# Optimization experiments

Measured on AMD Instinct MI355X. Metric: run time of the kernel, lower is better.

The kernel has to match this reference:

```python
import jax, jax.numpy as jnp
import numpy as np

jax.config.update("jax_enable_x64", True)  # torch lfilter runs in double precision

SR = 24000
RES_SIZE = 64
R_MIN, R_MAX = 0.9999, 0.99999
B, T = 4, 120000


def setup_inputs() -> dict:
    # Probe coefficients (fixed buffers, computed exactly as in Probe.__init__)
    theta_min = 2 * np.pi * 10.0 / SR
    theta_max = 2 * np.pi * 100.0 / SR
    theta = np.exp(np.linspace(np.log(theta_min), np.log(theta_max), RES_SIZE))
    radii = np.linspace(R_MIN, R_MAX, RES_SIZE)
    a1 = -2.0 * radii * np.cos(theta)          # [C]
    a2 = radii ** 2                             # [C]
    b0 = (1.0 - radii) * 0.5                    # [C]

    # Tank mixing weight: orthogonal init, shape [out=64, in=128] (rows orthonormal)
    rng = np.random.default_rng(1337)
    q, _ = np.linalg.qr(rng.standard_normal((2 * RES_SIZE, RES_SIZE)))  # [128,64], orthonormal cols
    W = q.T.astype(np.float32)                  # [64,128]

    key = jax.random.key(0)
    k1, k2 = jax.random.split(key)
    pred = jax.random.normal(k1, (B, 1, T), dtype=jnp.float32)
    target = jax.random.normal(k2, (B, 1, T), dtype=jnp.float32)
    return {
        "pred": pred,
        "target": target,
        "a1": jnp.asarray(a1, jnp.float64),
        "a2": jnp.asarray(a2, jnp.float64),
        "b0": jnp.asarray(b0, jnp.float64),
        "W": jnp.asarray(W, jnp.float32),
    }


def _biquad_bank(x, a1, a2, b0):
    """Biquad filter bank. x: [N, T] float64; coeffs: [C]. Returns [N, C, T].
    y[t] = b0*x[t] - a1*y[t-1] - a2*y[t-2]  (a0 = 1, b1 = b2 = 0, clamp=False)
    """
    n = x.shape[0]
    c = a1.shape[0]

    def step(carry, xt):
        y1, y2 = carry  # each [N, C]
        y = b0[None, :] * xt[:, None] - a1[None, :] * y1 - a2[None, :] * y2
        return (y, y1), y

    init = (jnp.zeros((n, c), x.dtype), jnp.zeros((n, c), x.dtype))
    _, ys = jax.lax.scan(step, init, x.T)      # [T, N, C]
    return jnp.transpose(ys, (1, 2, 0))        # [N, C, T]


def _probe(x, a1, a2, b0):
    """x: [B,1,T] float -> [B, 2C, T] float32 (fwd state ++ bwd state)."""
    xs = x[:, 0, :].astype(jnp.float64)        # [B, T]
    # run forward-time and reversed-time filters in one batched scan
    both = jnp.concatenate([xs, xs[:, ::-1]], axis=0)       # [2B, T]
    ys = _biquad_bank(both, a1, a2, b0)                      # [2B, C, T]
    nb = xs.shape[0]
    fwd_state = ys[:nb]                                      # [B, C, T]
    bwd_state = ys[nb:][:, :, ::-1]                          # [B, C, T] (flipped back)
    return jnp.concatenate([fwd_state, bwd_state], axis=1).astype(jnp.float32)


def _tank(x, W):
    """x: [B, 2C, T], W: [C, 2C] -> tanh(W @ x): [B, C, T]."""
    return jnp.tanh(jnp.einsum("bct,oc->bot", x, W))


def reference(pred, target, a1, a2, b0, W):
    t = pred.shape[-1]
    margin = t // 3
    p_emb = _tank(_probe(pred, a1, a2, b0), W)    # [B, C, T]
    t_emb = _tank(_probe(target, a1, a2, b0), W)  # [B, C, T]
    p_valid = p_emb[..., margin:t - margin]
    t_valid = t_emb[..., margin:t - margin]
    return jnp.mean(jnp.abs(p_valid - t_valid))
```

## Files before the change

### kernel.cpp

```cpp
#include <hip/hip_runtime.h>

#define T_LEN 120000
#define LBLK 160
#define PBLK 750
#define SEG_LEN 25
#define NSEG 30
#define CCH 32
#define NCHUNK (LBLK / CCH)
#define BATCH 4
#define K0 250
#define NKV 250
#define IB_LO 250
#define IB_HI 500
#define DENOM 20480000.0
#define YSTR 130

typedef _Float16 half8 __attribute__((ext_vector_type(8)));
typedef float f32x4 __attribute__((ext_vector_type(4)));

__device__ __forceinline__ float fast_tanh(float x) {
  float e = __expf(2.0f * x);
  return 1.0f - 2.0f / (e + 1.0f);
}

__device__ __forceinline__ void mat_pow(double A1, double A2, int e,
                                        double& r00, double& r01,
                                        double& r10, double& r11) {
  double m00 = -A1, m01 = -A2, m10 = 1.0, m11 = 0.0;
  r00 = 1.0; r01 = 0.0; r10 = 0.0; r11 = 1.0;
  while (e) {
    if (e & 1) {
      double t00 = r00 * m00 + r01 * m10, t01 = r00 * m01 + r01 * m11;
      double t10 = r10 * m00 + r11 * m10, t11 = r10 * m01 + r11 * m11;
      r00 = t00; r01 = t01; r10 = t10; r11 = t11;
    }
    e >>= 1;
    if (e) {
      double t00 = m00 * m00 + m01 * m10, t01 = m00 * m01 + m01 * m11;
      double t10 = m10 * m00 + m11 * m10, t11 = m10 * m01 + m11 * m11;
      m00 = t00; m01 = t01; m10 = t10; m11 = t11;
    }
  }
}

__global__ __launch_bounds__(256) void canon(
    const void* a1p, const void* a2p, const void* b0p, const float* __restrict__ W,
    double* ca1, double* ca2, double* cb0, float* cf, _Float16* Wh, double* wsum)
{
  int tid = threadIdx.x;
  __shared__ int isf64;
  if (tid == 0) {
    double probe = *(const double*)a2p;
    isf64 = (probe > 0.9 && probe < 1.0) ? 1 : 0;
    *wsum = 0.0;
  }
  __syncthreads();
  if (tid < 64) {
    double A1, A2, B0;
    if (isf64) {
      A1 = ((const double*)a1p)[tid];
      A2 = ((const double*)a2p)[tid];
      B0 = ((const double*)b0p)[tid];
    } else {
      A1 = (double)((const float*)a1p)[tid];
      A2 = (double)((const float*)a2p)[tid];
      B0 = (double)((const float*)b0p)[tid];
    }
    ca1[tid] = A1; ca2[tid] = A2; cb0[tid] = B0;
    cf[tid] = (float)A1; cf[64 + tid] = (float)A2;
    cf[128 + tid] = (float)B0; cf[192 + tid] = (float)(1.0 / A2);
  }
  for (int idx = tid; idx < 64 * 128; idx += 256) Wh[idx] = (_Float16)W[idx];
}

__global__ __launch_bounds__(64) void pass1(
    const float* __restrict__ pred, const float* __restrict__ tgt,
    const float* __restrict__ cf, double* __restrict__ fbuf)
{
  int k = blockIdx.x, r = blockIdx.y;
  int i = r >> 3, d = (r >> 2) & 1, b = r & 3;
  const float* sig = (i ? tgt : pred) + b * T_LEN;
  __shared__ float xs[LBLK];
  int base = k * LBLK;
  for (int j = threadIdx.x; j < LBLK; j += 64)
    xs[j] = d ? sig[T_LEN - 1 - (base + j)] : sig[base + j];
  __syncthreads();
  int ch = threadIdx.x;
  float A1 = cf[ch], A2 = cf[64 + ch], B0 = cf[128 + ch];
  float y1 = 0.0f, y2 = 0.0f;
  for (int j = 0; j < LBLK; ++j) {
    float y = fmaf(-A1, y1, fmaf(-A2, y2, B0 * xs[j]));
    y2 = y1; y1 = y;
  }
  int s = r * 64 + ch;
  ((double2*)fbuf)[(size_t)k * 1024 + s] = make_double2((double)y1, (double)y2);
}

__global__ __launch_bounds__(64) void pass2a(
    const double* __restrict__ a1, const double* __restrict__ a2,
    const double* __restrict__ fbuf, double* __restrict__ sbuf)
{
  int seg = blockIdx.x >> 4;
  int s = ((blockIdx.x & 15) << 6) + threadIdx.x;
  int ch = s & 63;
  double r00, r01, r10, r11;
  mat_pow(a1[ch], a2[ch], LBLK, r00, r01, r10, r11);
  const double2* fb = (const double2*)fbuf;
  double y1 = 0.0, y2 = 0.0;
  for (int jj = 0; jj < SEG_LEN / 5; ++jj) {
    size_t kb = (size_t)(seg * SEG_LEN + jj * 5) * 1024 + s;
    double2 f0 = fb[kb], f1 = fb[kb + 1024], f2 = fb[kb + 2048],
            f3 = fb[kb + 3072], f4 = fb[kb + 4096];
    double n1, n2;
    n1 = r00*y1 + r01*y2 + f0.x; n2 = r10*y1 + r11*y2 + f0.y; y1=n1; y2=n2;
    n1 = r00*y1 + r01*y2 + f1.x; n2 = r10*y1 + r11*y2 + f1.y; y1=n1; y2=n2;
    n1 = r00*y1 + r01*y2 + f2.x; n2 = r10*y1 + r11*y2 + f2.y; y1=n1; y2=n2;
    n1 = r00*y1 + r01*y2 + f3.x; n2 = r10*y1 + r11*y2 + f3.y; y1=n1; y2=n2;
    n1 = r00*y1 + r01*y2 + f4.x; n2 = r10*y1 + r11*y2 + f4.y; y1=n1; y2=n2;
  }
  ((double2*)sbuf)[(size_t)seg * 1024 + s] = make_double2(y1, y2);
}

__global__ __launch_bounds__(256) void pass2b(
    const double* __restrict__ a1, const double* __restrict__ a2,
    const double* __restrict__ sbuf, double* __restrict__ tbuf)
{
  int s = blockIdx.x * 256 + threadIdx.x;
  int ch = s & 63;
  double r00, r01, r10, r11;
  mat_pow(a1[ch], a2[ch], LBLK * SEG_LEN, r00, r01, r10, r11);
  const double2* sb = (const double2*)sbuf;
  double2* tb = (double2*)tbuf;
  double y1 = 0.0, y2 = 0.0;
  for (int seg = 0; seg < NSEG; ++seg) {
    tb[(size_t)seg * 1024 + s] = make_double2(y1, y2);
    double2 f = sb[(size_t)seg * 1024 + s];
    double n1 = r00 * y1 + r01 * y2 + f.x;
    double n2 = r10 * y1 + r11 * y2 + f.y;
    y1 = n1; y2 = n2;
  }
}

__global__ __launch_bounds__(64) void pass2c(
    const double* __restrict__ a1, const double* __restrict__ a2,
    const double* __restrict__ fbuf, const double* __restrict__ tbuf,
    double* __restrict__ ibuf)
{
  int seg = 10 + (blockIdx.x >> 4);
  int s = ((blockIdx.x & 15) << 6) + threadIdx.x;
  int ch = s & 63;
  double r00, r01, r10, r11;
  mat_pow(a1[ch], a2[ch], LBLK, r00, r01, r10, r11);
  const double2* fb = (const double2*)fbuf;
  double2* ib = (double2*)ibuf;
  double2 v = ((const double2*)tbuf)[(size_t)seg * 1024 + s];
  double y1 = v.x, y2 = v.y;
  for (int j = 0; j < SEG_LEN; ++j) {
    int k = seg * SEG_LEN + j;
    if (k >= IB_LO && k <= IB_HI)
      ib[(size_t)(k - IB_LO) * 1024 + s] = make_double2(y1, y2);
    double2 f = fb[(size_t)k * 1024 + s];
    double n1 = r00 * y1 + r01 * y2 + f.x;
    double n2 = r10 * y1 + r11 * y2 + f.y;
    y1 = n1; y2 = n2;
  }
}

__global__ __launch_bounds__(256, 4) void pass3(
    const float* __restrict__ pred, const float* __restrict__ tgt,
    const float* __restrict__ cf, const _Float16* __restrict__ Wh,
    const double* __restrict__ ibuf, double* __restrict__ wsum)
{
  int k = K0 + blockIdx.x;
  int b = blockIdx.y;
  int tid = threadIdx.x;
  __shared__ __align__(16) _Float16 ys[2][64 * YSTR];
  __shared__ float xs[2][LBLK];
  __shared__ float red[4];

  for (int idx = tid; idx < 2 * LBLK; idx += 256) {
    int ii = idx / LBLK, j = idx - ii * LBLK;
    const float* sig = (ii ? tgt : pred) + b * T_LEN;
    xs[ii][j] = sig[k * LBLK + j];
  }

  int g = tid >> 6, lane = tid & 63;
  int i = g >> 1, d = g & 1, ch = lane;
  int gu = __builtin_amdgcn_readfirstlane(g);
  int n0 = gu * 16;
  int lm = lane & 15, quad = lane >> 4;

  half8 wf[4][4];
  #pragma unroll
  for (int m0 = 0; m0 < 4; ++m0) {
    #pragma unroll
    for (int k0 = 0; k0 < 4; ++k0)
      wf[m0][k0] = *(const half8*)(Wh + (m0 * 16 + lm) * 128 + k0 * 32 + quad * 8);
  }

  int s = (i * 8 + d * 4 + b) * 64 + ch;
  float A1 = cf[ch], A2 = cf[64 + ch], B0 = cf[128 + ch], IA2 = cf[192 + ch];
  double2 v = (d == 0)
      ? ((const double2*)ibuf)[(size_t)(k - IB_LO) * 1024 + s]
      : ((const double2*)ibuf)[(size_t)(IB_HI - k) * 1024 + s];
  float st0 = (float)v.x, st1 = (float)v.y;
  __syncthreads();

  float loss = 0.0f;
  for (int cc = 0; cc < NCHUNK; ++cc) {
    _Float16* yb = ys[cc & 1];
    if (d == 0) {
      #pragma unroll
      for (int tt = 0; tt < CCH; ++tt) {
        float x = xs[i][cc * CCH + tt];
        float y = fmaf(-A1, st0, fmaf(-A2, st1, B0 * x));
        yb[(2 * tt + i) * YSTR + ch] = (_Float16)y;
        st1 = st0; st0 = y;
      }
    } else {
      #pragma unroll
      for (int tt = 0; tt < CCH; ++tt) {
        float x = xs[i][cc * CCH + tt];
        yb[(2 * tt + i) * YSTR + 64 + ch] = (_Float16)st0;
        float ym2 = (fmaf(-A1, st1, B0 * x) - st0) * IA2;
        st0 = st1; st1 = ym2;
      }
    }
    __syncthreads();

    const _Float16* yrow = &yb[(n0 + lm) * YSTR + quad * 8];
    half8 bf0 = *(const half8*)(yrow);
    half8 bf1 = *(const half8*)(yrow + 32);
    half8 bf2 = *(const half8*)(yrow + 64);
    half8 bf3 = *(const half8*)(yrow + 96);
    #pragma unroll
    for (int m0 = 0; m0 < 4; ++m0) {
      f32x4 c = {0.f, 0.f, 0.f, 0.f};
      c = __builtin_amdgcn_mfma_f32_16x16x32_f16(wf[m0][0], bf0, c, 0, 0, 0);
      c = __builtin_amdgcn_mfma_f32_16x16x32_f16(wf[m0][1], bf1, c, 0, 0, 0);
      c = __builtin_amdgcn_mfma_f32_16x16x32_f16(wf[m0][2], bf2, c, 0, 0, 0);
      c = __builtin_amdgcn_mfma_f32_16x16x32_f16(wf[m0][3], bf3, c, 0, 0, 0);
      #pragma unroll
      for (int r = 0; r < 4; ++r) {
        float vv = fast_tanh(c[r]);
        float p = __shfl_xor(vv, 1);
        loss += fabsf(vv - p);
      }
    }
  }

  #pragma unroll
  for (int off = 32; off > 0; off >>= 1) loss += __shfl_down(loss, off);
  if ((tid & 63) == 0) red[tid >> 6] = loss;
  __syncthreads();
  if (tid == 0) atomicAdd(wsum, (double)(red[0] + red[1] + red[2] + red[3]));
}

__global__ void finalize(const double* __restrict__ wsum, float* __restrict__ out) {
  out[0] = (float)(wsum[0] / DENOM);
}

extern "C" void kernel_launch(void* const* d_in, const int* in_sizes, int n_in,
                              void* d_out, int out_size, void* d_ws, size_t ws_size,
                              hipStream_t stream) {
  const float* pred = (const float*)d_in[0];
  const float* tgt  = (const float*)d_in[1];
  const float* W    = (const float*)d_in[5];
  float* out = (float*)d_out;

  double* base = (double*)d_ws;
  double* wsum = base;
  double* ca1  = base + 8;
  double* ca2  = base + 72;
  double* cb0  = base + 136;
  float*  cf   = (float*)(base + 200);
  _Float16* Wh = (_Float16*)(base + 328);
  double* fbuf = base + 2376;
  double* ibuf = fbuf + (size_t)PBLK * 1024 * 2;
  double* sbuf = ibuf + (size_t)(IB_HI - IB_LO + 1) * 1024 * 2;
  double* tbuf = sbuf + (size_t)NSEG * 1024 * 2;

  canon<<<1, 256, 0, stream>>>(d_in[2], d_in[3], d_in[4], W,
                               ca1, ca2, cb0, cf, Wh, wsum);
  pass1<<<dim3(PBLK, 16), 64, 0, stream>>>(pred, tgt, cf, fbuf);
  pass2a<<<NSEG * 16, 64, 0, stream>>>(ca1, ca2, fbuf, sbuf);
  pass2b<<<dim3(4), 256, 0, stream>>>(ca1, ca2, sbuf, tbuf);
  pass2c<<<11 * 16, 64, 0, stream>>>(ca1, ca2, fbuf, tbuf, ibuf);
  pass3<<<dim3(NKV, BATCH), 256, 0, stream>>>(pred, tgt, cf, Wh, ibuf, wsum);
  finalize<<<1, 1, 0, stream>>>(wsum, out);
}
```

Measured before the change: 137.1 us.

## Drop canon and pass2c kernels, fold state fix-up and coefficient conversion into pass3

Removes the coefficient canonicalisation kernel and the pass2c intermediate-state kernel. Each consumer now reads and converts the a1/a2/b0 coefficients itself, and pass3 rebuilds its starting state from the segment-start state plus up to 24 block-level matrix steps over fbuf. W is converted to fp16 directly inside pass3, and x is read from global memory instead of being staged in LDS. pass2b now batches its loads into two groups of 15. This cuts two kernel launches and their serial dependencies, at the cost of redundant per-block double-precision work in pass3 and uncoalesced-ish global x reads.

```diff
diff --git a/kernel.cpp b/kernel.cpp
--- a/kernel.cpp
+++ b/kernel.cpp
@@ -10,8 +10,6 @@
 #define BATCH 4
 #define K0 250
 #define NKV 250
-#define IB_LO 250
-#define IB_HI 500
 #define DENOM 20480000.0
 #define YSTR 130
 
@@ -21,6 +19,14 @@
 __device__ __forceinline__ float fast_tanh(float x) {
   float e = __expf(2.0f * x);
   return 1.0f - 2.0f / (e + 1.0f);
+}
+
+__device__ __forceinline__ bool coeffs_are_f64(const void* a2p) {
+  double probe = *(const double*)a2p;
+  return probe > 0.9 && probe < 1.0;
+}
+__device__ __forceinline__ double coeff_d(const void* p, bool f64, int ch) {
+  return f64 ? ((const double*)p)[ch] : (double)((const float*)p)[ch];
 }
 
 __device__ __forceinline__ void mat_pow(double A1, double A2, int e,
@@ -43,39 +49,10 @@
   }
 }
 
-__global__ __launch_bounds__(256) void canon(
-    const void* a1p, const void* a2p, const void* b0p, const float* __restrict__ W,
-    double* ca1, double* ca2, double* cb0, float* cf, _Float16* Wh, double* wsum)
-{
-  int tid = threadIdx.x;
-  __shared__ int isf64;
-  if (tid == 0) {
-    double probe = *(const double*)a2p;
-    isf64 = (probe > 0.9 && probe < 1.0) ? 1 : 0;
-    *wsum = 0.0;
-  }
-  __syncthreads();
-  if (tid < 64) {
-    double A1, A2, B0;
-    if (isf64) {
-      A1 = ((const double*)a1p)[tid];
-      A2 = ((const double*)a2p)[tid];
-      B0 = ((const double*)b0p)[tid];
-    } else {
-      A1 = (double)((const float*)a1p)[tid];
-      A2 = (double)((const float*)a2p)[tid];
-      B0 = (double)((const float*)b0p)[tid];
-    }
-    ca1[tid] = A1; ca2[tid] = A2; cb0[tid] = B0;
-    cf[tid] = (float)A1; cf[64 + tid] = (float)A2;
-    cf[128 + tid] = (float)B0; cf[192 + tid] = (float)(1.0 / A2);
-  }
-  for (int idx = tid; idx < 64 * 128; idx += 256) Wh[idx] = (_Float16)W[idx];
-}
-
 __global__ __launch_bounds__(64) void pass1(
     const float* __restrict__ pred, const float* __restrict__ tgt,
-    const float* __restrict__ cf, double* __restrict__ fbuf)
+    const void* a1p, const void* a2p, const void* b0p,
+    double* __restrict__ fbuf)
 {
   int k = blockIdx.x, r = blockIdx.y;
   int i = r >> 3, d = (r >> 2) & 1, b = r & 3;
@@ -86,7 +63,10 @@
     xs[j] = d ? sig[T_LEN - 1 - (base + j)] : sig[base + j];
   __syncthreads();
   int ch = threadIdx.x;
-  float A1 = cf[ch], A2 = cf[64 + ch], B0 = cf[128 + ch];
+  bool f64 = coeffs_are_f64(a2p);
+  float A1 = (float)coeff_d(a1p, f64, ch);
+  float A2 = (float)coeff_d(a2p, f64, ch);
+  float B0 = (float)coeff_d(b0p, f64, ch);
   float y1 = 0.0f, y2 = 0.0f;
   for (int j = 0; j < LBLK; ++j) {
     float y = fmaf(-A1, y1, fmaf(-A2, y2, B0 * xs[j]));
@@ -97,14 +77,15 @@
 }
 
 __global__ __launch_bounds__(64) void pass2a(
-    const double* __restrict__ a1, const double* __restrict__ a2,
+    const void* a1p, const void* a2p,
     const double* __restrict__ fbuf, double* __restrict__ sbuf)
 {
   int seg = blockIdx.x >> 4;
   int s = ((blockIdx.x & 15) << 6) + threadIdx.x;
   int ch = s & 63;
+  bool f64 = coeffs_are_f64(a2p);
   double r00, r01, r10, r11;
-  mat_pow(a1[ch], a2[ch], LBLK, r00, r01, r10, r11);
+  mat_pow(coeff_d(a1p, f64, ch), coeff_d(a2p, f64, ch), LBLK, r00, r01, r10, r11);
   const double2* fb = (const double2*)fbuf;
   double y1 = 0.0, y2 = 0.0;
   for (int jj = 0; jj < SEG_LEN / 5; ++jj) {
@@ -122,106 +103,117 @@
 }
 
 __global__ __launch_bounds__(256) void pass2b(
-    const double* __restrict__ a1, const double* __restrict__ a2,
+    const void* a1p, const void* a2p,
     const double* __restrict__ sbuf, double* __restrict__ tbuf)
 {
   int s = blockIdx.x * 256 + threadIdx.x;
   int ch = s & 63;
+  bool f64 = coeffs_are_f64(a2p);
   double r00, r01, r10, r11;
-  mat_pow(a1[ch], a2[ch], LBLK * SEG_LEN, r00, r01, r10, r11);
+  mat_pow(coeff_d(a1p, f64, ch), coeff_d(a2p, f64, ch), LBLK * SEG_LEN,
+          r00, r01, r10, r11);
   const double2* sb = (const double2*)sbuf;
   double2* tb = (double2*)tbuf;
   double y1 = 0.0, y2 = 0.0;
-  for (int seg = 0; seg < NSEG; ++seg) {
-    tb[(size_t)seg * 1024 + s] = make_double2(y1, y2);
-    double2 f = sb[(size_t)seg * 1024 + s];
-    double n1 = r00 * y1 + r01 * y2 + f.x;
-    double n2 = r10 * y1 + r11 * y2 + f.y;
-    y1 = n1; y2 = n2;
-  }
-}
-
-__global__ __launch_bounds__(64) void pass2c(
-    const double* __restrict__ a1, const double* __restrict__ a2,
-    const double* __restrict__ fbuf, const double* __restrict__ tbuf,
-    double* __restrict__ ibuf)
-{
-  int seg = 10 + (blockIdx.x >> 4);
-  int s = ((blockIdx.x & 15) << 6) + threadIdx.x;
-  int ch = s & 63;
-  double r00, r01, r10, r11;
-  mat_pow(a1[ch], a2[ch], LBLK, r00, r01, r10, r11);
-  const double2* fb = (const double2*)fbuf;
-  double2* ib = (double2*)ibuf;
-  double2 v = ((const double2*)tbuf)[(size_t)seg * 1024 + s];
-  double y1 = v.x, y2 = v.y;
-  for (int j = 0; j < SEG_LEN; ++j) {
-    int k = seg * SEG_LEN + j;
-    if (k >= IB_LO && k <= IB_HI)
-      ib[(size_t)(k - IB_LO) * 1024 + s] = make_double2(y1, y2);
-    double2 f = fb[(size_t)k * 1024 + s];
-    double n1 = r00 * y1 + r01 * y2 + f.x;
-    double n2 = r10 * y1 + r11 * y2 + f.y;
-    y1 = n1; y2 = n2;
+  #pragma unroll 1
+  for (int half = 0; half < 2; ++half) {
+    int base = half * 15;
+    double2 f[15];
+    #pragma unroll
+    for (int q = 0; q < 15; ++q) f[q] = sb[(size_t)(base + q) * 1024 + s];
+    #pragma unroll
+    for (int q = 0; q < 15; ++q) {
+      tb[(size_t)(base + q) * 1024 + s] = make_double2(y1, y2);
+      double n1 = r00 * y1 + r01 * y2 + f[q].x;
+      double n2 = r10 * y1 + r11 * y2 + f[q].y;
+      y1 = n1; y2 = n2;
+    }
   }
 }
 
 __global__ __launch_bounds__(256, 4) void pass3(
     const float* __restrict__ pred, const float* __restrict__ tgt,
-    const float* __restrict__ cf, const _Float16* __restrict__ Wh,
-    const double* __restrict__ ibuf, double* __restrict__ wsum)
+    const void* a1p, const void* a2p, const void* b0p,
+    const float* __restrict__ W, const double* __restrict__ fbuf,
+    const double* __restrict__ tbuf, double* __restrict__ wsum)
 {
   int k = K0 + blockIdx.x;
   int b = blockIdx.y;
   int tid = threadIdx.x;
   __shared__ __align__(16) _Float16 ys[2][64 * YSTR];
-  __shared__ float xs[2][LBLK];
   __shared__ float red[4];
 
-  for (int idx = tid; idx < 2 * LBLK; idx += 256) {
-    int ii = idx / LBLK, j = idx - ii * LBLK;
-    const float* sig = (ii ? tgt : pred) + b * T_LEN;
-    xs[ii][j] = sig[k * LBLK + j];
-  }
-
   int g = tid >> 6, lane = tid & 63;
-  int i = g >> 1, d = g & 1, ch = lane;
   int gu = __builtin_amdgcn_readfirstlane(g);
+  int iu = gu >> 1, du = gu & 1;
+  int ch = lane;
   int n0 = gu * 16;
   int lm = lane & 15, quad = lane >> 4;
+
+  bool f64 = coeffs_are_f64(a2p);
+  double A1d = coeff_d(a1p, f64, ch), A2d = coeff_d(a2p, f64, ch);
+  double B0d = coeff_d(b0p, f64, ch);
+  float A1 = (float)A1d, A2 = (float)A2d, B0 = (float)B0d;
+  float IA2 = (float)(1.0 / A2d);
+
+  int m = du ? (PBLK - k) : k;
+  int seg = m / SEG_LEN, j = m - seg * SEG_LEN;
+  int s = (iu * 8 + du * 4 + b) * 64 + ch;
+  double r00, r01, r10, r11;
+  mat_pow(A1d, A2d, LBLK, r00, r01, r10, r11);
+  double2 v0 = ((const double2*)tbuf)[(size_t)seg * 1024 + s];
+  double y1 = v0.x, y2 = v0.y;
+  const double2* fb = (const double2*)fbuf + (size_t)(seg * SEG_LEN) * 1024 + s;
+  #pragma unroll 1
+  for (int bb = 0; bb < 24; bb += 8) {
+    double2 f[8];
+    #pragma unroll
+    for (int q = 0; q < 8; ++q) f[q] = fb[(size_t)(bb + q) * 1024];
+    #pragma unroll
+    for (int q = 0; q < 8; ++q) {
+      if (bb + q < j) {
+        double n1 = r00 * y1 + r01 * y2 + f[q].x;
+        double n2 = r10 * y1 + r11 * y2 + f[q].y;
+        y1 = n1; y2 = n2;
+      }
+    }
+  }
+  float st0 = (float)y1, st1 = (float)y2;
 
   half8 wf[4][4];
   #pragma unroll
   for (int m0 = 0; m0 < 4; ++m0) {
     #pragma unroll
-    for (int k0 = 0; k0 < 4; ++k0)
-      wf[m0][k0] = *(const half8*)(Wh + (m0 * 16 + lm) * 128 + k0 * 32 + quad * 8);
-  }
-
-  int s = (i * 8 + d * 4 + b) * 64 + ch;
-  float A1 = cf[ch], A2 = cf[64 + ch], B0 = cf[128 + ch], IA2 = cf[192 + ch];
-  double2 v = (d == 0)
-      ? ((const double2*)ibuf)[(size_t)(k - IB_LO) * 1024 + s]
-      : ((const double2*)ibuf)[(size_t)(IB_HI - k) * 1024 + s];
-  float st0 = (float)v.x, st1 = (float)v.y;
-  __syncthreads();
+    for (int k0 = 0; k0 < 4; ++k0) {
+      const float* wp = W + (m0 * 16 + lm) * 128 + k0 * 32 + quad * 8;
+      float4 wa = *(const float4*)wp, wb = *(const float4*)(wp + 4);
+      half8 h;
+      h[0] = (_Float16)wa.x; h[1] = (_Float16)wa.y;
+      h[2] = (_Float16)wa.z; h[3] = (_Float16)wa.w;
+      h[4] = (_Float16)wb.x; h[5] = (_Float16)wb.y;
+      h[6] = (_Float16)wb.z; h[7] = (_Float16)wb.w;
+      wf[m0][k0] = h;
+    }
+  }
+
+  const float* xp = (iu ? tgt : pred) + b * T_LEN + k * LBLK;
 
   float loss = 0.0f;
   for (int cc = 0; cc < NCHUNK; ++cc) {
     _Float16* yb = ys[cc & 1];
-    if (d == 0) {
+    if (du == 0) {
       #pragma unroll
       for (int tt = 0; tt < CCH; ++tt) {
-        float x = xs[i][cc * CCH + tt];
+        float x = xp[cc * CCH + tt];
         float y = fmaf(-A1, st0, fmaf(-A2, st1, B0 * x));
-        yb[(2 * tt + i) * YSTR + ch] = (_Float16)y;
+        yb[(2 * tt + iu) * YSTR + ch] = (_Float16)y;
         st1 = st0; st0 = y;
       }
     } else {
       #pragma unroll
       for (int tt = 0; tt < CCH; ++tt) {
-        float x = xs[i][cc * CCH + tt];
-        yb[(2 * tt + i) * YSTR + 64 + ch] = (_Float16)st0;
+        float x = xp[cc * CCH + tt];
+        yb[(2 * tt + iu) * YSTR + 64 + ch] = (_Float16)st0;
         float ym2 = (fmaf(-A1, st1, B0 * x) - st0) * IA2;
         st0 = st1; st1 = ym2;
       }
@@ -265,27 +257,23 @@
                               hipStream_t stream) {
   const float* pred = (const float*)d_in[0];
   const float* tgt  = (const float*)d_in[1];
-  const float* W    = (const float*)d_in[5];
+  const void* a1p = d_in[2];
+  const void* a2p = d_in[3];
+  const void* b0p = d_in[4];
+  const float* W  = (const float*)d_in[5];
   float* out = (float*)d_out;
 
   double* base = (double*)d_ws;
   double* wsum = base;
-  double* ca1  = base + 8;
-  double* ca2  = base + 72;
-  double* cb0  = base + 136;
-  float*  cf   = (float*)(base + 200);
-  _Float16* Wh = (_Float16*)(base + 328);
-  double* fbuf = base + 2376;
-  double* ibuf = fbuf + (size_t)PBLK * 1024 * 2;
-  double* sbuf = ibuf + (size_t)(IB_HI - IB_LO + 1) * 1024 * 2;
+  double* fbuf = base + 8;
+  double* sbuf = fbuf + (size_t)PBLK * 1024 * 2;
   double* tbuf = sbuf + (size_t)NSEG * 1024 * 2;
 
-  canon<<<1, 256, 0, stream>>>(d_in[2], d_in[3], d_in[4], W,
-                               ca1, ca2, cb0, cf, Wh, wsum);
-  pass1<<<dim3(PBLK, 16), 64, 0, stream>>>(pred, tgt, cf, fbuf);
-  pass2a<<<NSEG * 16, 64, 0, stream>>>(ca1, ca2, fbuf, sbuf);
-  pass2b<<<dim3(4), 256, 0, stream>>>(ca1, ca2, sbuf, tbuf);
-  pass2c<<<11 * 16, 64, 0, stream>>>(ca1, ca2, fbuf, tbuf, ibuf);
-  pass3<<<dim3(NKV, BATCH), 256, 0, stream>>>(pred, tgt, cf, Wh, ibuf, wsum);
+  hipMemsetAsync(wsum, 0, sizeof(double), stream);
+  pass1<<<dim3(PBLK, 16), 64, 0, stream>>>(pred, tgt, a1p, a2p, b0p, fbuf);
+  pass2a<<<NSEG * 16, 64, 0, stream>>>(a1p, a2p, fbuf, sbuf);
+  pass2b<<<dim3(4), 256, 0, stream>>>(a1p, a2p, sbuf, tbuf);
+  pass3<<<dim3(NKV, BATCH), 256, 0, stream>>>(pred, tgt, a1p, a2p, b0p,
+                                              W, fbuf, tbuf, wsum);
   finalize<<<1, 1, 0, stream>>>(wsum, out);
 }
```

After: 128.0 us. 6.6% less time.
